# Optimization experiments

Hardware: AMD Instinct MI355X
Metric: run time of the kernel (lower is better)

## Reference

```python
import jax, jax.numpy as jnp
import numpy as np

N, T, HIDDEN = 32768, 2048, 128
NF = T // 2 + 1  # rfft bins


def setup_inputs() -> dict:
    key = jax.random.key(0)
    k1, k2, kw1, kw2 = jax.random.split(key, 4)
    x1 = jax.random.normal(k1, (N, T), dtype=jnp.float32)
    x2 = jax.random.normal(k2, (N, T), dtype=jnp.float32)
    # kaiming_uniform (relu): bound = sqrt(6 / fan_in)
    fan1 = 2 * NF
    W1 = jax.random.uniform(kw1, (HIDDEN, fan1), minval=-np.sqrt(6.0 / fan1), maxval=np.sqrt(6.0 / fan1), dtype=jnp.float32)
    b1 = jnp.zeros((HIDDEN,), dtype=jnp.float32)
    W2 = jax.random.uniform(kw2, (T, HIDDEN), minval=-np.sqrt(6.0 / HIDDEN), maxval=np.sqrt(6.0 / HIDDEN), dtype=jnp.float32)
    b2 = jnp.zeros((T,), dtype=jnp.float32)
    return {"x1": x1, "x2": x2, "W1": W1, "b1": b1, "W2": W2, "b2": b2}


def reference(x1, x2, W1, b1, W2, b2):
    # batched rfft replaces the per-sample Python loop
    diff = jnp.fft.rfft(x1, axis=-1) - jnp.fft.rfft(x2, axis=-1)  # [N, NF] complex
    feats = jnp.concatenate([diff.real, diff.imag], axis=-1)       # [N, 2*NF]
    h = jax.nn.relu(feats @ W1.T + b1)                             # [N, HIDDEN]
    out = h @ W2.T + b2                                            # [N, T]
    return jnp.mean(out, axis=-1)                                  # [N]
```

## Files before the change

kernel.cpp:

```cpp
#include <hip/hip_runtime.h>
#include <hip/hip_bf16.h>
#include <math.h>

#define T_LEN   2048
#define NFREQ   1025
#define HID     128
#define NSAMP   32768
#define NIT     64

typedef __attribute__((ext_vector_type(8)))  short short8v;
typedef __attribute__((ext_vector_type(16))) float f32x16;

#define AKG_OFF    0
#define W2BAR_OFF  (1u<<20)
#define B2BAR_OFF  ((1u<<20)+512)
#define PW_OFF     ((1u<<20)+1024)
#define PB_OFF     ((1u<<20)+1024+8192)

__global__ __launch_bounds__(128) void k_w2_partial(const float* __restrict__ W2,
                                                    const float* __restrict__ b2,
                                                    float* __restrict__ pw,
                                                    float* __restrict__ pb) {
    const int b = blockIdx.x;
    const int c = threadIdx.x;
    const int t0 = b * 128;
    float s0 = 0.f, s1 = 0.f, s2 = 0.f, s3 = 0.f;
    #pragma unroll 4
    for (int i = 0; i < 128; i += 4) {
        s0 += W2[(long)(t0 + i + 0) * HID + c];
        s1 += W2[(long)(t0 + i + 1) * HID + c];
        s2 += W2[(long)(t0 + i + 2) * HID + c];
        s3 += W2[(long)(t0 + i + 3) * HID + c];
    }
    pw[b * HID + c] = (s0 + s1) + (s2 + s3);
    float v = b2[t0 + c];
    for (int o = 32; o > 0; o >>= 1) v += __shfl_down(v, o);
    __shared__ float sred[2];
    if ((threadIdx.x & 63) == 0) sred[threadIdx.x >> 6] = v;
    __syncthreads();
    if (threadIdx.x == 0) pb[b] = sred[0] + sred[1];
}

__global__ __launch_bounds__(128) void k_w2_final(const float* __restrict__ pw,
                                                  const float* __restrict__ pb,
                                                  float* __restrict__ w2bar,
                                                  float* __restrict__ b2bar) {
    const int c = threadIdx.x;
    float s = 0.f;
    #pragma unroll
    for (int b = 0; b < 16; ++b) s += pw[b * HID + c];
    w2bar[c] = s * (1.f / (float)T_LEN);
    if (c == 0) {
        float t = 0.f;
        #pragma unroll
        for (int b = 0; b < 16; ++b) t += pb[b];
        *b2bar = t * (1.f / (float)T_LEN);
    }
}

__global__ __launch_bounds__(64) void k_build_At(const float* __restrict__ W1,
                                                 unsigned short* __restrict__ Akg) {
    const int k  = blockIdx.x >> 5;
    const int tc = blockIdx.x & 31;
    const int t  = tc * 64 + threadIdx.x;
    const float* __restrict__ Wr = W1 + (long)k * (2 * NFREQ);
    const float* __restrict__ Wi = Wr + NFREQ;
    const float w = -6.283185307179586f / (float)T_LEN;
    float sr, cr;
    sincosf(w * (float)t, &sr, &cr);
    float zr = 1.f, zi = 0.f;
    float acc = 0.f;
    int f = 0;
    for (int blk = 0; blk < 8; ++blk) {
        #pragma unroll 4
        for (int j = 0; j < 128; ++j) {
            acc = fmaf(Wr[f], zr, acc);
            acc = fmaf(Wi[f], zi, acc);
            float nzr = fmaf(zr, cr, -(zi * sr));
            float nzi = fmaf(zr, sr, zi * cr);
            zr = nzr; zi = nzi;
            ++f;
        }
        int ph = (t * f) & (T_LEN - 1);
        sincosf(w * (float)ph, &zi, &zr);
    }
    acc = fmaf(Wr[1024], zr, acc);
    acc = fmaf(Wi[1024], zi, acc);

    __hip_bfloat16 hb = __float2bfloat16(acc);
    float hf = __bfloat162float(hb);
    __hip_bfloat16 lb = __float2bfloat16(acc - hf);
    const int tile = t >> 5, inner = t & 31, islot = inner >> 3, j = t & 7;
    const int shi = islot ^ (k & 7);
    const int slo = (islot ^ 4) ^ (k & 7);
    const long base = (long)tile * 8192 + k * 64 + j;
    Akg[base + shi * 8] = __builtin_bit_cast(unsigned short, hb);
    Akg[base + slo * 8] = __builtin_bit_cast(unsigned short, lb);
}

__global__ __launch_bounds__(512) void k_gemm(const float* __restrict__ x1,
                                              const float* __restrict__ x2,
                                              const unsigned short* __restrict__ Akg,
                                              const float* __restrict__ b1,
                                              const float* __restrict__ w2bar,
                                              const float* __restrict__ b2bar,
                                              float* __restrict__ out) {
    __shared__ __align__(16) unsigned short ak[2][8192];
    __shared__ float osum[128];

    const int tid = threadIdx.x;
    const int l   = tid & 63;
    const int w   = tid >> 6;
    const int wm  = w & 3;
    const int wn  = w >> 2;
    const int g   = l >> 5;
    const int m31 = l & 31;
    const long row0 = (long)blockIdx.x * 128;

    const float* __restrict__ px1 = x1 + (row0 + wm * 32 + m31) * T_LEN + 8 * g;
    const float* __restrict__ px2 = x2 + (row0 + wm * 32 + m31) * T_LEN + 8 * g;
    const unsigned short* __restrict__ pak = Akg + w * 1024 + l * 8;

    f32x16 acc[2];
    #pragma unroll
    for (int tj = 0; tj < 2; ++tj)
        #pragma unroll
        for (int q = 0; q < 16; ++q) acc[tj][q] = 0.f;

    float4 xq[8];
    uint4  akr[2];

    {
        const float* p1 = px1; const float* p2 = px2;
        xq[0] = *(const float4*)(p1 + 0);  xq[1] = *(const float4*)(p1 + 4);
        xq[2] = *(const float4*)(p1 + 16); xq[3] = *(const float4*)(p1 + 20);
        xq[4] = *(const float4*)(p2 + 0);  xq[5] = *(const float4*)(p2 + 4);
        xq[6] = *(const float4*)(p2 + 16); xq[7] = *(const float4*)(p2 + 20);
        akr[0] = *(const uint4*)(pak + 0);
        akr[1] = *(const uint4*)(pak + 512);
    }

    for (int it = 0; it < NIT; ++it) {
        const int buf = it & 1;
        *(uint4*)&ak[buf][w * 1024 + l * 8]       = akr[0];
        *(uint4*)&ak[buf][w * 1024 + 512 + l * 8] = akr[1];

        short8v dh[2], dl[2];
        #pragma unroll
        for (int kc = 0; kc < 2; ++kc) {
            const float4 a0 = xq[2 * kc], a1 = xq[2 * kc + 1];
            const float4 b0 = xq[4 + 2 * kc], b1v = xq[5 + 2 * kc];
            float dv[8] = {a0.x - b0.x, a0.y - b0.y, a0.z - b0.z, a0.w - b0.w,
                           a1.x - b1v.x, a1.y - b1v.y, a1.z - b1v.z, a1.w - b1v.w};
            #pragma unroll
            for (int e = 0; e < 8; ++e) {
                __hip_bfloat16 hb = __float2bfloat16(dv[e]);
                float lo = dv[e] - __bfloat162float(hb);
                dh[kc][e] = __builtin_bit_cast(short, hb);
                dl[kc][e] = __builtin_bit_cast(short, __float2bfloat16(lo));
            }
        }

        if (it + 1 < NIT) {
            const float* p1 = px1 + (it + 1) * 32;
            const float* p2 = px2 + (it + 1) * 32;
            xq[0] = *(const float4*)(p1 + 0);  xq[1] = *(const float4*)(p1 + 4);
            xq[2] = *(const float4*)(p1 + 16); xq[3] = *(const float4*)(p1 + 20);
            xq[4] = *(const float4*)(p2 + 0);  xq[5] = *(const float4*)(p2 + 4);
            xq[6] = *(const float4*)(p2 + 16); xq[7] = *(const float4*)(p2 + 20);
            const unsigned short* pa = pak + (long)(it + 1) * 8192;
            akr[0] = *(const uint4*)(pa + 0);
            akr[1] = *(const uint4*)(pa + 512);
        }

        __syncthreads();

        #pragma unroll
        for (int kc = 0; kc < 2; ++kc) {
            #pragma unroll
            for (int tj = 0; tj < 2; ++tj) {
                const int r = wn * 64 + tj * 32 + m31;
                const int shi = ((2 * kc + g) ^ (r & 7)) * 8;
                const int slo = shi ^ 32;
                const short8v bh = *(const short8v*)&ak[buf][r * 64 + shi];
                const short8v bl = *(const short8v*)&ak[buf][r * 64 + slo];
                acc[tj] = __builtin_amdgcn_mfma_f32_32x32x16_bf16(dh[kc], bh, acc[tj], 0, 0, 0);
                acc[tj] = __builtin_amdgcn_mfma_f32_32x32x16_bf16(dh[kc], bl, acc[tj], 0, 0, 0);
                acc[tj] = __builtin_amdgcn_mfma_f32_32x32x16_bf16(dl[kc], bh, acc[tj], 0, 0, 0);
            }
        }
    }

    float pres[16];
    #pragma unroll
    for (int q = 0; q < 16; ++q) pres[q] = 0.f;
    #pragma unroll
    for (int tj = 0; tj < 2; ++tj) {
        const int n = wn * 64 + tj * 32 + m31;
        const float bb1 = b1[n], wb = w2bar[n];
        #pragma unroll
        for (int q = 0; q < 16; ++q)
            pres[q] += fmaxf(acc[tj][q] + bb1, 0.f) * wb;
    }
    #pragma unroll
    for (int q = 0; q < 16; ++q) {
        float s = pres[q];
        s += __shfl_xor(s, 1); s += __shfl_xor(s, 2); s += __shfl_xor(s, 4);
        s += __shfl_xor(s, 8); s += __shfl_xor(s, 16);
        pres[q] = s;
    }
    __syncthreads();
    if (wn == 0 && m31 == 0) {
        #pragma unroll
        for (int q = 0; q < 16; ++q)
            osum[wm * 32 + (q & 3) + 8 * (q >> 2) + 4 * g] = pres[q];
    }
    __syncthreads();
    if (wn == 1 && m31 == 0) {
        const float bb = *b2bar;
        #pragma unroll
        for (int q = 0; q < 16; ++q) {
            const int m = wm * 32 + (q & 3) + 8 * (q >> 2) + 4 * g;
            out[row0 + m] = pres[q] + osum[m] + bb;
        }
    }
}

extern "C" void kernel_launch(void* const* d_in, const int* in_sizes, int n_in,
                              void* d_out, int out_size, void* d_ws, size_t ws_size,
                              hipStream_t stream) {
    const float* x1 = (const float*)d_in[0];
    const float* x2 = (const float*)d_in[1];
    const float* W1 = (const float*)d_in[2];
    const float* b1 = (const float*)d_in[3];
    const float* W2 = (const float*)d_in[4];
    const float* b2 = (const float*)d_in[5];
    float* out = (float*)d_out;

    char* ws = (char*)d_ws;
    unsigned short* Akg = (unsigned short*)(ws + AKG_OFF);
    float* w2bar = (float*)(ws + W2BAR_OFF);
    float* b2bar = (float*)(ws + B2BAR_OFF);
    float* pw    = (float*)(ws + PW_OFF);
    float* pb    = (float*)(ws + PB_OFF);

    hipLaunchKernelGGL(k_w2_partial, dim3(16), dim3(128), 0, stream, W2, b2, pw, pb);
    hipLaunchKernelGGL(k_w2_final,   dim3(1),  dim3(128), 0, stream, pw, pb, w2bar, b2bar);
    hipLaunchKernelGGL(k_build_At,   dim3(4096), dim3(64), 0, stream, W1, Akg);
    hipLaunchKernelGGL(k_gemm,       dim3(NSAMP / 128), dim3(512), 0, stream,
                       x1, x2, Akg, b1, w2bar, b2bar, out);
}
```

Before: 671.5 us.

## Stage x-difference tiles in LDS and split DFT-matrix build across frequency halves

In the GEMM, each thread now loads a contiguous 32-float slice of one row of x1/x2, converts the difference to split-bf16 once, and writes it to a swizzled LDS buffer. MFMA A-operands are then read from LDS instead of being built by every wave from strided global reads, which removes the duplicate x loads and conversions across the two wn waves. The W1-transform kernel caches the W1 row in LDS and splits the frequency sum between lane halves, combining them with a shuffle, to gain more parallelism per output. This costs extra LDS capacity and traffic in the GEMM.

```diff
diff --git a/kernel.cpp b/kernel.cpp
--- a/kernel.cpp
+++ b/kernel.cpp
@@ -58,44 +58,60 @@
     }
 }
 
-__global__ __launch_bounds__(64) void k_build_At(const float* __restrict__ W1,
-                                                 unsigned short* __restrict__ Akg) {
-    const int k  = blockIdx.x >> 5;
-    const int tc = blockIdx.x & 31;
-    const int t  = tc * 64 + threadIdx.x;
-    const float* __restrict__ Wr = W1 + (long)k * (2 * NFREQ);
-    const float* __restrict__ Wi = Wr + NFREQ;
+__global__ __launch_bounds__(256) void k_build_At(const float* __restrict__ W1,
+                                                  unsigned short* __restrict__ Akg) {
+    __shared__ float lW[2 * NFREQ];
+    const int k  = blockIdx.x >> 4;
+    const int tg = blockIdx.x & 15;
+    const int tid = threadIdx.x;
+    const float* __restrict__ Wk = W1 + (long)k * (2 * NFREQ);
+    for (int i = tid; i < 2 * NFREQ; i += 256) lW[i] = Wk[i];
+    __syncthreads();
+    const float* __restrict__ lWr = lW;
+    const float* __restrict__ lWi = lW + NFREQ;
+
+    const int chunk = tid >> 6;
+    const int fh = (tid >> 5) & 1;
+    const int tl = tid & 31;
+    const int t  = tg * 128 + chunk * 32 + tl;
+
     const float w = -6.283185307179586f / (float)T_LEN;
     float sr, cr;
-    sincosf(w * (float)t, &sr, &cr);
-    float zr = 1.f, zi = 0.f;
+    { int ph2 = (2 * t) & (T_LEN - 1); sincosf(w * (float)ph2, &sr, &cr); }
+    float zr, zi;
+    { int ph = (t * fh) & (T_LEN - 1); sincosf(w * (float)ph, &zi, &zr); }
     float acc = 0.f;
-    int f = 0;
-    for (int blk = 0; blk < 8; ++blk) {
+    int f = fh;
+    for (int blk = 0; blk < 4; ++blk) {
         #pragma unroll 4
         for (int j = 0; j < 128; ++j) {
-            acc = fmaf(Wr[f], zr, acc);
-            acc = fmaf(Wi[f], zi, acc);
+            acc = fmaf(lWr[f], zr, acc);
+            acc = fmaf(lWi[f], zi, acc);
             float nzr = fmaf(zr, cr, -(zi * sr));
             float nzi = fmaf(zr, sr, zi * cr);
             zr = nzr; zi = nzi;
-            ++f;
+            f += 2;
         }
         int ph = (t * f) & (T_LEN - 1);
         sincosf(w * (float)ph, &zi, &zr);
     }
-    acc = fmaf(Wr[1024], zr, acc);
-    acc = fmaf(Wi[1024], zi, acc);
-
-    __hip_bfloat16 hb = __float2bfloat16(acc);
-    float hf = __bfloat162float(hb);
-    __hip_bfloat16 lb = __float2bfloat16(acc - hf);
-    const int tile = t >> 5, inner = t & 31, islot = inner >> 3, j = t & 7;
-    const int shi = islot ^ (k & 7);
-    const int slo = (islot ^ 4) ^ (k & 7);
-    const long base = (long)tile * 8192 + k * 64 + j;
-    Akg[base + shi * 8] = __builtin_bit_cast(unsigned short, hb);
-    Akg[base + slo * 8] = __builtin_bit_cast(unsigned short, lb);
+    if (fh == 0) {
+        acc = fmaf(lWr[1024], zr, acc);
+        acc = fmaf(lWi[1024], zi, acc);
+    }
+    acc += __shfl_xor(acc, 32);
+
+    if (fh == 0) {
+        __hip_bfloat16 hb = __float2bfloat16(acc);
+        float hf = __bfloat162float(hb);
+        __hip_bfloat16 lb = __float2bfloat16(acc - hf);
+        const int tile = t >> 5, islot = (t & 31) >> 3, j = t & 7;
+        const int shi = islot ^ (k & 7);
+        const int slo = (islot ^ 4) ^ (k & 7);
+        const long base = (long)tile * 8192 + k * 64 + j;
+        Akg[base + shi * 8] = __builtin_bit_cast(unsigned short, hb);
+        Akg[base + slo * 8] = __builtin_bit_cast(unsigned short, lb);
+    }
 }
 
 __global__ __launch_bounds__(512) void k_gemm(const float* __restrict__ x1,
@@ -106,6 +122,7 @@
                                               const float* __restrict__ b2bar,
                                               float* __restrict__ out) {
     __shared__ __align__(16) unsigned short ak[2][8192];
+    __shared__ __align__(16) unsigned short dd[2][8192];
     __shared__ float osum[128];
 
     const int tid = threadIdx.x;
@@ -117,9 +134,16 @@
     const int m31 = l & 31;
     const long row0 = (long)blockIdx.x * 128;
 
-    const float* __restrict__ px1 = x1 + (row0 + wm * 32 + m31) * T_LEN + 8 * g;
-    const float* __restrict__ px2 = x2 + (row0 + wm * 32 + m31) * T_LEN + 8 * g;
-    const unsigned short* __restrict__ pak = Akg + w * 1024 + l * 8;
+    const int rs = tid >> 2;
+    const int j4 = tid & 3;
+    const float* __restrict__ px1 = x1 + (row0 + rs) * T_LEN + j4 * 8;
+    const float* __restrict__ px2 = x2 + (row0 + rs) * T_LEN + j4 * 8;
+    const unsigned short* __restrict__ pak = Akg + tid * 16;
+
+    const int wr_hi = rs * 64 + ((j4 ^ (rs & 7)) * 8);
+    const int ra  = wm * 32 + m31;
+    const int rb0 = wn * 64 + m31;
+    const int rb1 = wn * 64 + 32 + m31;
 
     f32x16 acc[2];
     #pragma unroll
@@ -127,66 +151,54 @@
         #pragma unroll
         for (int q = 0; q < 16; ++q) acc[tj][q] = 0.f;
 
-    float4 xq[8];
-    uint4  akr[2];
-
-    {
-        const float* p1 = px1; const float* p2 = px2;
-        xq[0] = *(const float4*)(p1 + 0);  xq[1] = *(const float4*)(p1 + 4);
-        xq[2] = *(const float4*)(p1 + 16); xq[3] = *(const float4*)(p1 + 20);
-        xq[4] = *(const float4*)(p2 + 0);  xq[5] = *(const float4*)(p2 + 4);
-        xq[6] = *(const float4*)(p2 + 16); xq[7] = *(const float4*)(p2 + 20);
-        akr[0] = *(const uint4*)(pak + 0);
-        akr[1] = *(const uint4*)(pak + 512);
-    }
+    float4 xa0, xa1, xb0, xb1;
+    uint4  akr0, akr1;
+    xa0 = *(const float4*)(px1);     xa1 = *(const float4*)(px1 + 4);
+    xb0 = *(const float4*)(px2);     xb1 = *(const float4*)(px2 + 4);
+    akr0 = *(const uint4*)(pak);     akr1 = *(const uint4*)(pak + 8);
 
     for (int it = 0; it < NIT; ++it) {
         const int buf = it & 1;
-        *(uint4*)&ak[buf][w * 1024 + l * 8]       = akr[0];
-        *(uint4*)&ak[buf][w * 1024 + 512 + l * 8] = akr[1];
-
-        short8v dh[2], dl[2];
-        #pragma unroll
-        for (int kc = 0; kc < 2; ++kc) {
-            const float4 a0 = xq[2 * kc], a1 = xq[2 * kc + 1];
-            const float4 b0 = xq[4 + 2 * kc], b1v = xq[5 + 2 * kc];
-            float dv[8] = {a0.x - b0.x, a0.y - b0.y, a0.z - b0.z, a0.w - b0.w,
-                           a1.x - b1v.x, a1.y - b1v.y, a1.z - b1v.z, a1.w - b1v.w};
-            #pragma unroll
-            for (int e = 0; e < 8; ++e) {
-                __hip_bfloat16 hb = __float2bfloat16(dv[e]);
-                float lo = dv[e] - __bfloat162float(hb);
-                dh[kc][e] = __builtin_bit_cast(short, hb);
-                dl[kc][e] = __builtin_bit_cast(short, __float2bfloat16(lo));
-            }
-        }
+        float dv[8] = {xa0.x - xb0.x, xa0.y - xb0.y, xa0.z - xb0.z, xa0.w - xb0.w,
+                       xa1.x - xb1.x, xa1.y - xb1.y, xa1.z - xb1.z, xa1.w - xb1.w};
+        short8v dhv, dlv;
+        #pragma unroll
+        for (int e = 0; e < 8; ++e) {
+            __hip_bfloat16 hb = __float2bfloat16(dv[e]);
+            float lo = dv[e] - __bfloat162float(hb);
+            dhv[e] = __builtin_bit_cast(short, hb);
+            dlv[e] = __builtin_bit_cast(short, __float2bfloat16(lo));
+        }
+        *(short8v*)&dd[buf][wr_hi]      = dhv;
+        *(short8v*)&dd[buf][wr_hi ^ 32] = dlv;
+        *(uint4*)&ak[buf][tid * 16]     = akr0;
+        *(uint4*)&ak[buf][tid * 16 + 8] = akr1;
 
         if (it + 1 < NIT) {
             const float* p1 = px1 + (it + 1) * 32;
             const float* p2 = px2 + (it + 1) * 32;
-            xq[0] = *(const float4*)(p1 + 0);  xq[1] = *(const float4*)(p1 + 4);
-            xq[2] = *(const float4*)(p1 + 16); xq[3] = *(const float4*)(p1 + 20);
-            xq[4] = *(const float4*)(p2 + 0);  xq[5] = *(const float4*)(p2 + 4);
-            xq[6] = *(const float4*)(p2 + 16); xq[7] = *(const float4*)(p2 + 20);
+            xa0 = *(const float4*)(p1);     xa1 = *(const float4*)(p1 + 4);
+            xb0 = *(const float4*)(p2);     xb1 = *(const float4*)(p2 + 4);
             const unsigned short* pa = pak + (long)(it + 1) * 8192;
-            akr[0] = *(const uint4*)(pa + 0);
-            akr[1] = *(const uint4*)(pa + 512);
+            akr0 = *(const uint4*)(pa);     akr1 = *(const uint4*)(pa + 8);
         }
 
         __syncthreads();
 
         #pragma unroll
         for (int kc = 0; kc < 2; ++kc) {
+            const int sa = ((2 * kc + g) ^ (ra & 7)) * 8;
+            const short8v ah = *(const short8v*)&dd[buf][ra * 64 + sa];
+            const short8v al = *(const short8v*)&dd[buf][ra * 64 + (sa ^ 32)];
             #pragma unroll
             for (int tj = 0; tj < 2; ++tj) {
-                const int r = wn * 64 + tj * 32 + m31;
-                const int shi = ((2 * kc + g) ^ (r & 7)) * 8;
-                const int slo = shi ^ 32;
-                const short8v bh = *(const short8v*)&ak[buf][r * 64 + shi];
-                const short8v bl = *(const short8v*)&ak[buf][r * 64 + slo];
-                acc[tj] = __builtin_amdgcn_mfma_f32_32x32x16_bf16(dh[kc], bh, acc[tj], 0, 0, 0);
-                acc[tj] = __builtin_amdgcn_mfma_f32_32x32x16_bf16(dh[kc], bl, acc[tj], 0, 0, 0);
-                acc[tj] = __builtin_amdgcn_mfma_f32_32x32x16_bf16(dl[kc], bh, acc[tj], 0, 0, 0);
+                const int r = (tj == 0) ? rb0 : rb1;
+                const int sb = ((2 * kc + g) ^ (r & 7)) * 8;
+                const short8v bh = *(const short8v*)&ak[buf][r * 64 + sb];
+                const short8v bl = *(const short8v*)&ak[buf][r * 64 + (sb ^ 32)];
+                acc[tj] = __builtin_amdgcn_mfma_f32_32x32x16_bf16(ah, bh, acc[tj], 0, 0, 0);
+                acc[tj] = __builtin_amdgcn_mfma_f32_32x32x16_bf16(ah, bl, acc[tj], 0, 0, 0);
+                acc[tj] = __builtin_amdgcn_mfma_f32_32x32x16_bf16(al, bh, acc[tj], 0, 0, 0);
             }
         }
     }
@@ -246,7 +258,7 @@
 
     hipLaunchKernelGGL(k_w2_partial, dim3(16), dim3(128), 0, stream, W2, b2, pw, pb);
     hipLaunchKernelGGL(k_w2_final,   dim3(1),  dim3(128), 0, stream, pw, pb, w2bar, b2bar);
-    hipLaunchKernelGGL(k_build_At,   dim3(4096), dim3(64), 0, stream, W1, Akg);
+    hipLaunchKernelGGL(k_build_At,   dim3(2048), dim3(256), 0, stream, W1, Akg);
     hipLaunchKernelGGL(k_gemm,       dim3(NSAMP / 128), dim3(512), 0, stream,
                        x1, x2, Akg, b1, w2bar, b2bar, out);
 }
```

New measurement: 566.8 us. 1.18x faster.
